# Performance work log

Hardware: AMD Instinct MI355X
Metric: run time of the kernel (lower is better)

## Reference

```python
import jax, jax.numpy as jnp
import numpy as np

B, L, D, NLAYERS, MAX_NODES, DEG = 32, 512, 768, 3, 128, 8


def _build_graph():
    rng = np.random.default_rng(0)
    per = rng.integers(-32, 33, size=B // 2)
    sizes = np.concatenate([96 + per, 96 - per]).astype(np.int64)  # sum = 96*B = 3072, each in [64,128]
    N = int(sizes.sum())
    offs = np.concatenate([[0], np.cumsum(sizes)])
    batch = np.repeat(np.arange(B), sizes).astype(np.int64)
    pad_idx = np.zeros((B, MAX_NODES), np.int64)
    pad_mask = np.zeros((B, MAX_NODES), bool)
    src, dst = [], []
    for b in range(B):
        n = int(sizes[b])
        pad_idx[b, :n] = np.arange(offs[b], offs[b] + n)
        pad_mask[b, :n] = True
        src.append(rng.integers(offs[b], offs[b] + n, n * DEG))
        dst.append(rng.integers(offs[b], offs[b] + n, n * DEG))
    return N, batch, pad_idx, pad_mask, np.concatenate(src), np.concatenate(dst)


def setup_inputs() -> dict:
    N, batch, pad_idx, pad_mask, esrc, edst = _build_graph()
    key = jax.random.key(0)
    ks = jax.random.split(key, 8)
    s = 1.0 / np.sqrt(D)
    return {
        "x": jax.random.normal(ks[0], (N, D), jnp.float32),
        "text": jax.random.normal(ks[1], (B, L, D), jnp.float32),
        "batch_ent1_d_mask": jnp.ones((B, 1), jnp.float32),
        "batch_ent1_g_mask": jnp.ones((B, 1), jnp.float32),
        "gnn_ws": jax.random.normal(ks[2], (NLAYERS, D, D), jnp.float32) * s,
        "gnn_wn": jax.random.normal(ks[3], (NLAYERS, D, D), jnp.float32) * s,
        "gnn_b": jnp.zeros((NLAYERS, D), jnp.float32),
        "atom_w": jax.random.normal(ks[4], (D, D), jnp.float32) * s,
        "atom_b": jnp.zeros((D,), jnp.float32),
        "rand_emb": jax.random.normal(ks[5], (1, D), jnp.float32),
        "batch": jnp.asarray(batch),
        "pad_idx": jnp.asarray(pad_idx),
        "pad_mask": jnp.asarray(pad_mask),
        "edge_src": jnp.asarray(esrc),
        "edge_dst": jnp.asarray(edst),
    }


def reference(x, text, batch_ent1_d_mask, batch_ent1_g_mask, gnn_ws, gnn_wn, gnn_b,
              atom_w, atom_b, rand_emb, batch, pad_idx, pad_mask, edge_src, edge_dst):
    N = x.shape[0]
    E = edge_src.shape[0]
    maskf = pad_mask.astype(x.dtype)            # [B, M]
    n_per = maskf.sum(axis=1)                   # [B] num real nodes per graph
    # edge-neighbor mean counts (constants w.r.t. x)
    cnt = jax.ops.segment_sum(jnp.ones((E,), x.dtype), edge_dst, num_segments=N)
    inv_cnt = 1.0 / jnp.maximum(cnt, 1.0)
    cms = []
    for i in range(NLAYERS):
        # MoleGraphConv stand-in: mean neighbor aggregation + self transform
        msg = jax.ops.segment_sum(x[edge_src], edge_dst, num_segments=N) * inv_cnt[:, None]
        x = jax.nn.relu(x @ gnn_ws[i] + msg @ gnn_wn[i] + gnn_b[i])
        # ragged gather into padded [B, M, D]
        xp = x[pad_idx] * maskf[..., None]
        # graph -> text cross attention (softmax over text tokens; no mask needed)
        g2t = jax.nn.softmax(jnp.einsum('bmd,bld->bml', xp, text), axis=-1)
        g2t_out = jnp.einsum('bml,bld->bmd', g2t, text)            # [B, M, D]
        # text -> graph cross attention (mask padded nodes)
        t2g_logits = jnp.einsum('bld,bmd->blm', text, xp)
        t2g_logits = jnp.where(pad_mask[:, None, :], t2g_logits, jnp.float32(-1e9))
        t2g = jax.nn.softmax(t2g_logits, axis=-1)
        t2g_out = jnp.einsum('blm,bmd->bld', t2g, xp)              # [B, L, D]
        # mean over concatenated rows [n_i + L] per graph (pool_type=2)
        pooled = ((g2t_out * maskf[..., None]).sum(axis=1) + t2g_out.sum(axis=1)) \
                 / (n_per + jnp.float32(L))[:, None]
        cms.append(pooled)
    out_cms = jnp.mean(jnp.stack(cms, axis=1), axis=1)              # mean over layers
    out_t = text[:, 0, :]
    # scatter-mean of final node features per graph
    gsum = jax.ops.segment_sum(x, batch, num_segments=B)
    gcnt = jax.ops.segment_sum(jnp.ones((N,), x.dtype), batch, num_segments=B)
    xg = gsum / jnp.maximum(gcnt, 1.0)[:, None]
    # dropout is a no-op in eval mode
    out_g = jnp.tanh(xg @ atom_w + atom_b)
    z = rand_emb[0]
    dg = batch_ent1_d_mask * batch_ent1_g_mask
    return jnp.concatenate([
        out_t * batch_ent1_d_mask + (1 - batch_ent1_d_mask) * z,
        out_g * batch_ent1_g_mask + (1 - batch_ent1_g_mask) * z,
        out_cms * dg + (1 - dg) * z,
    ], axis=-1)
```

## Files before the change

### kernel.cpp

```cpp
#include <hip/hip_runtime.h>

#define D 768
#define B 32
#define L 512
#define M 128
#define NNODES 3072
#define NEDGES 24576

using bf16x8 = __attribute__((ext_vector_type(8))) short;
using f32x4  = __attribute__((ext_vector_type(4))) float;

__device__ __forceinline__ float bf2f(unsigned short u) {
  union { unsigned int i; float f; } v; v.i = ((unsigned int)u) << 16; return v.f;
}
__device__ __forceinline__ unsigned short f2bf(float f) {
  union { float f; unsigned int i; } v; v.f = f;
  unsigned int x = v.i;
  return (unsigned short)((x + 0x7FFFu + ((x >> 16) & 1u)) >> 16);
}
__device__ __forceinline__ float ldf(const void* p, size_t i, int f32) {
  return f32 ? ((const float*)p)[i] : bf2f(((const unsigned short*)p)[i]);
}
__device__ __forceinline__ int ldi(const void* p, size_t i, int w64) {
  return w64 ? (int)((const long long*)p)[i] : ((const int*)p)[i];
}
__device__ __forceinline__ f32x4 mfma16(bf16x8 a, bf16x8 b, f32x4 c) {
  return __builtin_amdgcn_mfma_f32_16x16x32_bf16(a, b, c, 0, 0, 0);
}
__device__ __forceinline__ void gl_lds(const unsigned short* gsrc, unsigned short* lbase,
                                       int lane) {
  __builtin_amdgcn_global_load_lds(
      (const __attribute__((address_space(1))) unsigned int*)(gsrc + lane * 8),
      (__attribute__((address_space(3))) unsigned int*)lbase, 16, 0, 0);
}

__device__ __forceinline__ float pk_read(const unsigned short* P, int p, int l, int d) {
  return bf2f(P[(((size_t)(p * 24 + (d >> 5))) << 9) + ((((d & 31) >> 3) << 4) + l) * 8 + (d & 7)]);
}

__device__ __forceinline__ void fma8(float* acc, float w, uint4 v) {
  unsigned xs[4] = {v.x, v.y, v.z, v.w};
#pragma unroll
  for (int j = 0; j < 4; ++j) {
    acc[2 * j]     += w * bf2f((unsigned short)(xs[j] & 0xFFFFu));
    acc[2 * j + 1] += w * bf2f((unsigned short)(xs[j] >> 16));
  }
}

__device__ __forceinline__ void acc12(float* a, const uint2* u) {
#pragma unroll
  for (int j = 0; j < 3; ++j) {
    a[j * 4 + 0] += bf2f((unsigned short)(u[j].x & 0xFFFFu));
    a[j * 4 + 1] += bf2f((unsigned short)(u[j].x >> 16));
    a[j * 4 + 2] += bf2f((unsigned short)(u[j].y & 0xFFFFu));
    a[j * 4 + 3] += bf2f((unsigned short)(u[j].y >> 16));
  }
}


__device__ void d_pack_in(const void* src, unsigned short* rows, unsigned short* dst,
                          int p, int tid, int f) {
  unsigned short* pb = dst + (size_t)p * 12288;
  uint4 qv[6];
  if (f) {
    float4 v0[6], v1[6];
#pragma unroll
    for (int j = 0; j < 6; ++j) {
      int odx = j * 256 + tid;
      int kk = odx >> 6, lanep = odx & 63;
      size_t sbase = (size_t)(p * 16 + (lanep & 15)) * 768 + kk * 32 + ((lanep >> 4) << 3);
      const float* sp = (const float*)src + sbase;
      v0[j] = *(const float4*)sp;
      v1[j] = *(const float4*)(sp + 4);
    }
#pragma unroll
    for (int j = 0; j < 6; ++j) {
      union { unsigned short v[8]; uint4 q; } u;
      u.v[0] = f2bf(v0[j].x); u.v[1] = f2bf(v0[j].y); u.v[2] = f2bf(v0[j].z); u.v[3] = f2bf(v0[j].w);
      u.v[4] = f2bf(v1[j].x); u.v[5] = f2bf(v1[j].y); u.v[6] = f2bf(v1[j].z); u.v[7] = f2bf(v1[j].w);
      qv[j] = u.q;
    }
  } else {
#pragma unroll
    for (int j = 0; j < 6; ++j) {
      int odx = j * 256 + tid;
      int kk = odx >> 6, lanep = odx & 63;
      size_t sbase = (size_t)(p * 16 + (lanep & 15)) * 768 + kk * 32 + ((lanep >> 4) << 3);
      qv[j] = *(const uint4*)((const unsigned short*)src + sbase);
    }
  }
#pragma unroll
  for (int j = 0; j < 6; ++j) {
    int odx = j * 256 + tid;
    int kk = odx >> 6, lanep = odx & 63;
    size_t sbase = (size_t)(p * 16 + (lanep & 15)) * 768 + kk * 32 + ((lanep >> 4) << 3);
    if (rows) *(uint4*)&rows[sbase] = qv[j];
    *(uint4*)&pb[(size_t)odx * 8] = qv[j];
  }
}

__device__ void d_pack(const unsigned short* src, unsigned short* dst,
                       int p, int tid) {
  unsigned short* pb = dst + (size_t)p * 12288;
  uint4 qv[6];
#pragma unroll
  for (int j = 0; j < 6; ++j) {
    int odx = j * 256 + tid;
    int kk = odx >> 6, lanep = odx & 63;
    size_t sbase = (size_t)(p * 16 + (lanep & 15)) * 768 + kk * 32 + ((lanep >> 4) << 3);
    qv[j] = *(const uint4*)(src + sbase);
  }
#pragma unroll
  for (int j = 0; j < 6; ++j) {
    *(uint4*)&pb[(size_t)(j * 256 + tid) * 8] = qv[j];
  }
}

__device__ void d_wpack(const void* Ws, const void* Wn, const void* Aw, int f,
                        unsigned short* WsPk, unsigned short* WnPk, unsigned short* AwPk,
                        int r0, int tid) {
  int z = r0 / 288, rem = r0 % 288;
  int nblk = rem % 12, kk = rem / 12;
  const void* src; unsigned short* dst; size_t zoff;
  if (z < 3)      { src = Ws; zoff = (size_t)z * D * D;       dst = WsPk + zoff; }
  else if (z < 6) { src = Wn; zoff = (size_t)(z - 3) * D * D; dst = WnPk + zoff; }
  else            { src = Aw; zoff = 0;                       dst = AwPk; }
  int pl = tid >> 6, lane = tid & 63;
  int pG = nblk * 4 + pl;
  int k0 = kk * 32 + ((lane >> 4) << 3);
  int n  = nblk * 64 + pl * 16 + (lane & 15);
  union { unsigned short v[8]; uint4 q; } u;
  if (f) {
    const float* sp = (const float*)src + zoff + (size_t)k0 * D + n;
#pragma unroll
    for (int e = 0; e < 8; ++e) u.v[e] = f2bf(sp[(size_t)e * D]);
  } else {
    const unsigned short* sp = (const unsigned short*)src + zoff + (size_t)k0 * D + n;
#pragma unroll
    for (int e = 0; e < 8; ++e) u.v[e] = sp[(size_t)e * D];
  }
  *(uint4*)&dst[(((size_t)(pG * 24 + kk)) << 9) + lane * 8] = u.q;
}

__device__ void d_count(const void* edst, const void* batch, int w,
                        int* cnt, int* gcnt, int i) {
  if (i < NEDGES) atomicAdd(&cnt[ldi(edst, i, w)], 1);
  if (i < NNODES) atomicAdd(&gcnt[ldi(batch, i, w)], 1);
}

__device__ void d_msg(const unsigned short* x, const int* cnt, const int* rowstart,
                      const int* csr, unsigned short* Mpk, int p, int tid) {
  int w = tid >> 6, lane = tid & 63;
  unsigned short* pb = Mpk + (size_t)p * 12288;
#pragma unroll
  for (int i = 0; i < 4; i += 2) {
    int rA = w * 4 + i, rB = rA + 1;
    int nA = p * 16 + rA, nB = p * 16 + rB;
    int degA = cnt[nA], baseA = rowstart[nA];
    int degB = cnt[nB], baseB = rowstart[nB];
    float aA[12], aB[12];
#pragma unroll
    for (int j = 0; j < 12; ++j) { aA[j] = 0.f; aB[j] = 0.f; }
    int dmax = degA > degB ? degA : degB;
    for (int e = 0; e < dmax; ++e) {
      uint2 uA[3], uB[3];
      if (e < degA) {
        const uint2* xr = (const uint2*)(x + (size_t)csr[baseA + e] * D);
        uA[0] = xr[lane]; uA[1] = xr[lane + 64]; uA[2] = xr[lane + 128];
      }
      if (e < degB) {
        const uint2* xr = (const uint2*)(x + (size_t)csr[baseB + e] * D);
        uB[0] = xr[lane]; uB[1] = xr[lane + 64]; uB[2] = xr[lane + 128];
      }
      if (e < degA) acc12(aA, uA);
      if (e < degB) acc12(aB, uB);
    }
    float invA = 1.0f / (float)(degA > 1 ? degA : 1);
    float invB = 1.0f / (float)(degB > 1 ? degB : 1);
#pragma unroll
    for (int j = 0; j < 3; ++j) {
      int d0 = (lane + j * 64) * 4;
      int kk = d0 >> 5, q = (d0 >> 3) & 3, e0 = d0 & 7;
      uint2 wA, wB;
      wA.x = (unsigned int)f2bf(aA[j * 4 + 0] * invA)
           | ((unsigned int)f2bf(aA[j * 4 + 1] * invA) << 16);
      wA.y = (unsigned int)f2bf(aA[j * 4 + 2] * invA)
           | ((unsigned int)f2bf(aA[j * 4 + 3] * invA) << 16);
      wB.x = (unsigned int)f2bf(aB[j * 4 + 0] * invB)
           | ((unsigned int)f2bf(aB[j * 4 + 1] * invB) << 16);
      wB.y = (unsigned int)f2bf(aB[j * 4 + 2] * invB)
           | ((unsigned int)f2bf(aB[j * 4 + 3] * invB) << 16);
      *(uint2*)&pb[kk * 512 + (q * 16 + rA) * 8 + e0] = wA;
      *(uint2*)&pb[kk * 512 + (q * 16 + rB) * 8 + e0] = wB;
    }
  }
}

__device__ void d_gemm(const unsigned short* Xpk, const unsigned short* Mpk,
                       const unsigned short* WsPk, const unsigned short* WnPk,
                       const void* bias, size_t bias_off, int f,
                       unsigned short* Y, int bx, int by, int tid, char* smem) {
  unsigned short* lds = (unsigned short*)smem;
  int wave = tid >> 6, lane = tid & 63;
  int q = lane >> 4, t = lane & 15;
  int wm = wave >> 1, wn = wave & 1;
  int pa = bx * 4, pb = by * 4;
  f32x4 acc[2][2];
#pragma unroll
  for (int mi = 0; mi < 2; ++mi)
#pragma unroll
    for (int ni = 0; ni < 2; ++ni)
      acc[mi][ni] = (f32x4){0.f, 0.f, 0.f, 0.f};
  int c0 = wave * 2;
  int pan0 = (wave < 2) ? (pa + c0) : (pb + c0 - 4);
  auto issue = [&](int r) {
    unsigned short* dbuf = &lds[(r % 3) * 8192 + c0 * 512];
#pragma unroll
    for (int st = 0; st < 2; ++st) {
      int s = r * 2 + st;
      int h = (s >= 24) ? 1 : 0;
      const unsigned short* P = (wave < 2) ? (h ? Mpk : Xpk) : (h ? WnPk : WsPk);
      int kk = s - h * 24;
      gl_lds(P + (((size_t)(pan0 * 24 + kk)) << 9), dbuf + st * 4096, lane);
      gl_lds(P + (((size_t)((pan0 + 1) * 24 + kk)) << 9), dbuf + st * 4096 + 512, lane);
    }
  };
  issue(0);
  issue(1);
  for (int r = 0; r < 24; ++r) {
    if (r < 23) asm volatile("s_waitcnt vmcnt(4)" ::: "memory");
    else        asm volatile("s_waitcnt vmcnt(0)" ::: "memory");
    __builtin_amdgcn_s_barrier();
    asm volatile("" ::: "memory");
    if (r < 22) issue(r + 2);
    const unsigned short* bb = &lds[(r % 3) * 8192];
#pragma unroll
    for (int st = 0; st < 2; ++st) {
      const unsigned short* bs = bb + st * 4096;
      bf16x8 a0 = *(const bf16x8*)&bs[(wm * 2 + 0) * 512 + lane * 8];
      bf16x8 a1 = *(const bf16x8*)&bs[(wm * 2 + 1) * 512 + lane * 8];
      bf16x8 b0 = *(const bf16x8*)&bs[(4 + wn * 2 + 0) * 512 + lane * 8];
      bf16x8 b1 = *(const bf16x8*)&bs[(4 + wn * 2 + 1) * 512 + lane * 8];
      acc[0][0] = mfma16(a0, b0, acc[0][0]);
      acc[0][1] = mfma16(a0, b1, acc[0][1]);
      acc[1][0] = mfma16(a1, b0, acc[1][0]);
      acc[1][1] = mfma16(a1, b1, acc[1][1]);
    }
    asm volatile("" ::: "memory");
  }
#pragma unroll
  for (int ni = 0; ni < 2; ++ni) {
    int col = by * 64 + wn * 32 + ni * 16 + t;
    float bv = ldf(bias, bias_off + col, f);
#pragma unroll
    for (int mi = 0; mi < 2; ++mi) {
#pragma unroll
      for (int r = 0; r < 4; ++r) {
        int row = bx * 64 + wm * 32 + mi * 16 + q * 4 + r;
        float v = acc[mi][ni][r] + bv;
        Y[(size_t)row * D + col] = f2bf(v > 0.f ? v : 0.f);
      }
    }
  }
}

__device__ void d_xp(const unsigned short* Xn, const void* pidx, int w64,
                     const int* gcnt, unsigned short* xp, unsigned short* XpPk,
                     float* xgacc, int p, int tid, char* smem) {
  unsigned short* rows = (unsigned short*)smem;
  int r = tid >> 4, c16 = tid & 15;
  int bm = p * 16 + r;
  int b = bm >> 7, m = bm & 127;
  int nb = gcnt[b];
  uint4* dl = (uint4*)&rows[r * 776];
  uint4 v[6];
  if (m < nb) {
    const uint4* srcr = (const uint4*)(Xn + (size_t)ldi(pidx, bm, w64) * D);
#pragma unroll
    for (int j = 0; j < 6; ++j) v[j] = srcr[c16 + j * 16];
  } else {
    uint4 z = {0u, 0u, 0u, 0u};
#pragma unroll
    for (int j = 0; j < 6; ++j) v[j] = z;
  }
#pragma unroll
  for (int j = 0; j < 6; ++j) dl[c16 + j * 16] = v[j];
  __syncthreads();
#pragma unroll
  for (int j = 0; j < 6; ++j) {
    int idx = j * 256 + tid;
    int rr = idx / 96, cc = idx % 96;
    uint4 vv = *(const uint4*)&rows[rr * 776 + cc * 8];
    *(uint4*)&xp[(size_t)(p * 16 + rr) * D + cc * 8] = vv;
  }
  unsigned short* pb = XpPk + (size_t)p * 12288;
#pragma unroll
  for (int j = 0; j < 6; ++j) {
    int odx = j * 256 + tid;
    int kk = odx >> 6, lanep = odx & 63;
    int rr = lanep & 15, cg = lanep >> 4;
    int cc = kk * 4 + cg;
    uint4 vv = *(const uint4*)&rows[rr * 776 + cc * 8];
    *(uint4*)&pb[odx * 8] = vv;
  }
  if (xgacc) {
    int bb = p >> 3;
#pragma unroll
    for (int j = 0; j < 3; ++j) {
      int d = j * 256 + tid;
      float s = 0.f;
#pragma unroll
      for (int rr = 0; rr < 16; ++rr) s += bf2f(rows[rr * 776 + d]);
      atomicAdd(&xgacc[(size_t)bb * D + d], s);
    }
  }
}

__device__ void d_scores(const unsigned short* XpPk, const unsigned short* Tpk,
                         float* S, int bx, int by, int bz, int tid, char* smem) {
  unsigned short* lds = (unsigned short*)smem;
  int wave = tid >> 6, lane = tid & 63;
  int q = lane >> 4, t = lane & 15;
  int wm = wave >> 1, wn = wave & 1;
  int pa = bz * 8 + bx * 4;
  int pb = bz * 32 + by * 4;
  f32x4 acc[2][2];
#pragma unroll
  for (int mi = 0; mi < 2; ++mi)
#pragma unroll
    for (int ni = 0; ni < 2; ++ni)
      acc[mi][ni] = (f32x4){0.f, 0.f, 0.f, 0.f};
  int c0 = wave * 2;
  const unsigned short* P = (wave < 2) ? XpPk : Tpk;
  int pan0 = (wave < 2) ? (pa + c0) : (pb + c0 - 4);
  auto issue = [&](int r) {
    unsigned short* dbuf = &lds[(r % 3) * 8192 + c0 * 512];
#pragma unroll
    for (int st = 0; st < 2; ++st) {
      int kk = r * 2 + st;
      gl_lds(P + (((size_t)(pan0 * 24 + kk)) << 9), dbuf + st * 4096, lane);
      gl_lds(P + (((size_t)((pan0 + 1) * 24 + kk)) << 9), dbuf + st * 4096 + 512, lane);
    }
  };
  issue(0);
  issue(1);
  for (int r = 0; r < 12; ++r) {
    if (r < 11) asm volatile("s_waitcnt vmcnt(4)" ::: "memory");
    else        asm volatile("s_waitcnt vmcnt(0)" ::: "memory");
    __builtin_amdgcn_s_barrier();
    asm volatile("" ::: "memory");
    if (r < 10) issue(r + 2);
    const unsigned short* bb = &lds[(r % 3) * 8192];
#pragma unroll
    for (int st = 0; st < 2; ++st) {
      const unsigned short* bs = bb + st * 4096;
      bf16x8 a0 = *(const bf16x8*)&bs[(wm * 2 + 0) * 512 + lane * 8];
      bf16x8 a1 = *(const bf16x8*)&bs[(wm * 2 + 1) * 512 + lane * 8];
      bf16x8 b0 = *(const bf16x8*)&bs[(4 + wn * 2 + 0) * 512 + lane * 8];
      bf16x8 b1 = *(const bf16x8*)&bs[(4 + wn * 2 + 1) * 512 + lane * 8];
      acc[0][0] = mfma16(a0, b0, acc[0][0]);
      acc[0][1] = mfma16(a0, b1, acc[0][1]);
      acc[1][0] = mfma16(a1, b0, acc[1][0]);
      acc[1][1] = mfma16(a1, b1, acc[1][1]);
    }
    asm volatile("" ::: "memory");
  }
  float* Sb = S + (size_t)bz * M * L;
#pragma unroll
  for (int ni = 0; ni < 2; ++ni) {
    int col = by * 64 + wn * 32 + ni * 16 + t;
#pragma unroll
    for (int mi = 0; mi < 2; ++mi) {
#pragma unroll
      for (int r = 0; r < 4; ++r) {
        int row = bx * 64 + wm * 32 + mi * 16 + q * 4 + r;
        Sb[(size_t)row * L + col] = acc[mi][ni][r];
      }
    }
  }
}

__device__ void d_stats(const float* S, const int* gcnt, float* rmax, float* rsum,
                        float* cmaxv, float* csumv, int bid, int tid, char* smem) {
  if (bid < B * M) {
    float* red = (float*)smem;
    int lane = tid & 63, wv = tid >> 6;
    const float* r = S + (size_t)bid * L;
    float s0 = r[tid], s1 = r[tid + 256];
    float m = fmaxf(s0, s1);
#pragma unroll
    for (int o = 32; o > 0; o >>= 1) m = fmaxf(m, __shfl_down(m, o));
    if (lane == 0) red[wv] = m;
    __syncthreads();
    float bm = fmaxf(fmaxf(red[0], red[1]), fmaxf(red[2], red[3]));
    __syncthreads();
    float e = __expf(s0 - bm) + __expf(s1 - bm);
#pragma unroll
    for (int o = 32; o > 0; o >>= 1) e += __shfl_down(e, o);
    if (lane == 0) red[wv] = e;
    __syncthreads();
    if (tid == 0) { rmax[bid] = bm; rsum[bid] = red[0] + red[1] + red[2] + red[3]; }
  } else {
    float (*pm)[64] = (float(*)[64])smem;
    float (*ps)[64] = (float(*)[64])(smem + 1024);
    int cid = bid - B * M;
    int b = cid >> 3, ly = cid & 7;
    int w = tid >> 6, lane = tid & 63;
    int l = ly * 64 + lane;
    int nb = gcnt[b];
    const float* Sb = S + (size_t)b * M * L;
    int m0 = w * 32, m1 = min(m0 + 32, nb);
    float cm = -1e30f, cs = 0.f;
    for (int m = m0; m < m1; ++m) {
      float s = Sb[(size_t)m * L + l];
      if (s > cm) { cs = cs * __expf(cm - s) + 1.f; cm = s; }
      else cs += __expf(s - cm);
    }
    pm[w][lane] = cm; ps[w][lane] = cs;
    __syncthreads();
    if (w == 0) {
      float CM = -1e30f;
#pragma unroll
      for (int j = 0; j < 4; ++j) CM = fmaxf(CM, pm[j][lane]);
      float CS = 0.f;
#pragma unroll
      for (int j = 0; j < 4; ++j) CS += ps[j][lane] * __expf(pm[j][lane] - CM);
      cmaxv[b * L + l] = CM; csumv[b * L + l] = CS;
    }
  }
}

__device__ void d_cross(const float* S, const float* rmax, const float* rsum,
                        const float* cmaxv, const float* csumv, const int* gcnt,
                        float* wv, float* t2gcol, int bid, int tid, char* smem) {
  if (bid < 256) {
    float* rm = (float*)smem;
    float* ri = (float*)(smem + 512);
    float (*pw)[64] = (float(*)[64])(smem + 1024);
    int b = bid >> 3, ly = bid & 7;
    int w = tid >> 6, lane = tid & 63;
    if (tid < M) { rm[tid] = rmax[b * M + tid]; ri[tid] = 1.f / rsum[b * M + tid]; }
    __syncthreads();
    int l = ly * 64 + lane;
    int nb = gcnt[b];
    const float* Sb = S + (size_t)b * M * L;
    int m0 = w * 32, m1 = min(m0 + 32, nb);
    float wp = 0.f;
    for (int m = m0; m < m1; ++m)
      wp += __expf(Sb[(size_t)m * L + l] - rm[m]) * ri[m];
    pw[w][lane] = wp;
    __syncthreads();
    if (w == 0)
      wv[b * L + l] = pw[0][lane] + pw[1][lane] + pw[2][lane] + pw[3][lane];
  } else {
    float* red = (float*)smem;
    int bm = bid - 256;
    int b = bm >> 7, m = bm & 127;
    int lane = tid & 63, w = tid >> 6;
    int nb = gcnt[b];
    float acc = 0.f;
    if (m < nb) {
      const float* r = S + (size_t)bm * L;
      const float* cm = cmaxv + b * L;
      const float* cs = csumv + b * L;
      acc = __expf(r[tid] - cm[tid]) / cs[tid]
          + __expf(r[tid + 256] - cm[tid + 256]) / cs[tid + 256];
    }
#pragma unroll
    for (int o = 32; o > 0; o >>= 1) acc += __shfl_down(acc, o);
    if (lane == 0) red[w] = acc;
    __syncthreads();
    if (tid == 0) t2gcol[bm] = red[0] + red[1] + red[2] + red[3];
  }
}

__device__ void d_pooled(const float* wv, const float* t2gcol, const unsigned short* Tpk,
                         const unsigned short* xp, const int* gcnt, float* pooled,
                         int bid, int tid, char* smem) {
  float* lred = (float*)smem;
  float* wbuf = (float*)(smem + 3072);
  int b = bid / 10, seg = bid - b * 10;
  int chunk = tid % 96, half = tid / 96;
  int d = chunk * 8;
  float acc[8];
#pragma unroll
  for (int j = 0; j < 8; ++j) acc[j] = 0.f;
  if (tid < 64) {
    wbuf[tid] = (seg < 8) ? wv[b * L + seg * 64 + tid]
                          : t2gcol[b * M + (seg - 8) * 64 + tid];
  }
  __syncthreads();
  if (half < 2) {
    if (seg < 8) {
      int pbase = b * 32 + seg * 4;
      size_t cbase = ((size_t)(d >> 5)) << 9;
      int coff = ((d & 31) >> 3) << 4;
      for (int i = 0; i < 32; ++i) {
        int l = half * 32 + i;
        const unsigned short* src =
            Tpk + (((size_t)((pbase + (l >> 4)) * 24)) << 9) + cbase +
            (size_t)(coff + (l & 15)) * 8;
        fma8(acc, wbuf[l], *(const uint4*)src);
      }
    } else {
      const unsigned short* Xb = xp + (size_t)b * M * D + d;
      int m0 = (seg - 8) * 64;
      for (int i = 0; i < 32; ++i) {
        int mm = half * 32 + i;
        fma8(acc, wbuf[mm], *(const uint4*)&Xb[(size_t)(m0 + mm) * D]);
      }
    }
  }
  if (half == 1) {
#pragma unroll
    for (int j = 0; j < 8; ++j) lred[chunk * 8 + j] = acc[j];
  }
  __syncthreads();
  if (half == 0) {
    float inv = 1.f / ((float)gcnt[b] + 512.f);
#pragma unroll
    for (int j = 0; j < 8; ++j)
      atomicAdd(&pooled[(size_t)b * D + d + j], (acc[j] + lred[chunk * 8 + j]) * inv);
  }
}

__device__ void d_atom(const float* xgacc, const int* gcnt, const unsigned short* AwPk,
                       float* gpre, int bid, int tid) {
  int w = tid >> 6, lane = tid & 63;
  int q = lane >> 4, t = lane & 15;
  int nbase = bid * 64 + w * 16;
  int pb = nbase >> 4;
  int n0 = gcnt[t], n1 = gcnt[16 + t];
  float inv0 = 1.f / (float)(n0 > 1 ? n0 : 1);
  float inv1 = 1.f / (float)(n1 > 1 ? n1 : 1);
  f32x4 acc[2];
  acc[0] = (f32x4){0.f, 0.f, 0.f, 0.f};
  acc[1] = (f32x4){0.f, 0.f, 0.f, 0.f};
  for (int kk = 0; kk < 24; ++kk) {
    const float* s0 = xgacc + (size_t)t * D + kk * 32 + q * 8;
    const float* s1 = xgacc + (size_t)(16 + t) * D + kk * 32 + q * 8;
    union { unsigned short v[8]; bf16x8 f; } a0, a1;
#pragma unroll
    for (int j = 0; j < 8; ++j) { a0.v[j] = f2bf(s0[j] * inv0); a1.v[j] = f2bf(s1[j] * inv1); }
    bf16x8 bv = *(const bf16x8*)(AwPk + (((size_t)(pb * 24 + kk)) << 9) + (lane << 3));
    acc[0] = mfma16(a0.f, bv, acc[0]);
    acc[1] = mfma16(a1.f, bv, acc[1]);
  }
#pragma unroll
  for (int mi = 0; mi < 2; ++mi)
#pragma unroll
    for (int r = 0; r < 4; ++r) {
      int row = mi * 16 + q * 4 + r;
      gpre[(size_t)row * D + nbase + t] = acc[mi][r];
    }
}


__global__ void k_init(int* cnt, int* cursor, int* gcnt, float* pooled, float* xgacc,
                       const unsigned short* __restrict__ t,
                       const unsigned int* __restrict__ e, int* __restrict__ flags) {
  int i = blockIdx.x * 256 + threadIdx.x;
  if (i < NNODES) { cnt[i] = 0; cursor[i] = 0; }
  if (i < B) gcnt[i] = 0;
  if (i < B * D) { pooled[i] = 0.f; xgacc[i] = 0.f; }
  if (blockIdx.x == 0) {
    __shared__ int r0[256];
    __shared__ unsigned r1[256];
    int tid = threadIdx.x;
    int bad = 0;
    for (int j = tid; j < 8192; j += 256) {
      unsigned short u = t[2 * j];
      unsigned ex = (u >> 7) & 0xFF;
      if (ex >= 0xC0) bad = 1;
    }
    unsigned o = 0;
    for (int j = tid; j < NEDGES / 2; j += 256) o |= e[2 * j + 1];
    r0[tid] = bad; r1[tid] = o;
    __syncthreads();
    for (int s = 128; s > 0; s >>= 1) {
      if (tid < s) { r0[tid] |= r0[tid + s]; r1[tid] |= r1[tid + s]; }
      __syncthreads();
    }
    if (tid == 0) { flags[0] = r0[0]; flags[1] = (r1[0] == 0) ? 1 : 0; }
  }
}

__global__ __launch_bounds__(256) void k_setup2(
    const void* x_in, unsigned short* x0, unsigned short* PkA,
    const void* text, unsigned short* Tpk,
    const void* Ws, const void* Wn, const void* Aw,
    unsigned short* WsPk, unsigned short* WnPk, unsigned short* AwPk,
    const void* edst, const void* batch, int* cnt, int* gcnt,
    const int* __restrict__ flags) {
  int bid = blockIdx.x, tid = threadIdx.x;
  if (bid < 1216) {
    int f = flags[0];
    if (bid < NNODES / 16) d_pack_in(x_in, x0, PkA, bid, tid, f);
    else d_pack_in(text, nullptr, Tpk, bid - NNODES / 16, tid, f);
  } else if (bid < 3232) {
    d_wpack(Ws, Wn, Aw, flags[0], WsPk, WnPk, AwPk, bid - 1216, tid);
  } else {
    d_count(edst, batch, flags[1], cnt, gcnt, (bid - 3232) * 256 + tid);
  }
}

__global__ void k_scan(const int* __restrict__ cnt, int* __restrict__ rowstart) {
  __shared__ int a[NNODES], b[NNODES];
  int tid = threadIdx.x;
  for (int i = tid; i < NNODES; i += 1024) a[i] = cnt[i];
  __syncthreads();
  int* s = a; int* d = b;
  for (int off = 1; off < NNODES; off <<= 1) {
    for (int i = tid; i < NNODES; i += 1024)
      d[i] = s[i] + (i >= off ? s[i - off] : 0);
    __syncthreads();
    int* t = s; s = d; d = t;
  }
  for (int i = tid; i < NNODES; i += 1024) rowstart[i + 1] = s[i];
  if (tid == 0) rowstart[0] = 0;
}

__global__ void k_scatter(const void* __restrict__ esrc, const void* __restrict__ edst,
                          const int* __restrict__ flags, const int* __restrict__ rowstart,
                          int* __restrict__ cursor, int* __restrict__ csr) {
  int w = flags[1];
  int i = blockIdx.x * 256 + threadIdx.x;
  if (i < NEDGES) {
    int dd = ldi(edst, i, w);
    int pos = atomicAdd(&cursor[dd], 1);
    csr[rowstart[dd] + pos] = ldi(esrc, i, w);
  }
}

__global__ __launch_bounds__(256) void k_msgp(
    const unsigned short* x, const int* cnt, const int* rowstart, const int* csr,
    unsigned short* Mpk) {
  d_msg(x, cnt, rowstart, csr, Mpk, blockIdx.x, threadIdx.x);
}

__device__ __forceinline__ void gemm_map(int g, int& bx, int& by) {
  int gs = (g % 8) * 72 + g / 8;
  bx = gs / 12; by = gs % 12;
}
__device__ __forceinline__ void sc_map(int g, int& bx, int& by, int& bz) {
  int gs = (g % 8) * 64 + g / 8;
  bx = gs & 1; by = (gs >> 1) & 7; bz = gs >> 4;
}

__global__ __launch_bounds__(256) void k_gemm(
    const unsigned short* Apk, const unsigned short* Mpk,
    const unsigned short* WsPk, const unsigned short* WnPk,
    const void* bias, unsigned long bias_off, const int* flags, unsigned short* Y) {
  extern __shared__ char smem[];
  int bx, by; gemm_map(blockIdx.x, bx, by);
  d_gemm(Apk, Mpk, WsPk, WnPk, bias, bias_off, flags[0], Y, bx, by,
         threadIdx.x, smem);
}

__global__ __launch_bounds__(256) void k_postg(
    const unsigned short* Y, unsigned short* Npk, int packN,
    const void* pidx, const int* flags, const int* gcnt,
    unsigned short* xp, unsigned short* XpPk, float* xgacc) {
  extern __shared__ char smem[];
  int bid = blockIdx.x, tid = threadIdx.x;
  if (bid < 256) d_xp(Y, pidx, flags[1], gcnt, xp, XpPk, xgacc, bid, tid, smem);
  else d_pack(Y, Npk, bid - 256, tid);
}

__global__ __launch_bounds__(256) void k_scmsg(
    const unsigned short* XpPk, const unsigned short* Tpk, float* S,
    int msgN, const unsigned short* x, const int* cnt, const int* rowstart,
    const int* csr, unsigned short* Mpk) {
  extern __shared__ char smem[];
  int bid = blockIdx.x, tid = threadIdx.x;
  if (bid < msgN) d_msg(x, cnt, rowstart, csr, Mpk, bid, tid);
  else {
    int bx, by, bz; sc_map(bid - msgN, bx, by, bz);
    d_scores(XpPk, Tpk, S, bx, by, bz, tid, smem);
  }
}

__global__ __launch_bounds__(256) void k_stgemm(
    const float* S, const int* gcnt, float* rmax, float* rsum, float* cmaxv, float* csumv,
    int gemmN, const unsigned short* Apk, const unsigned short* Mpk,
    const unsigned short* WsPk, const unsigned short* WnPk,
    const void* bias, unsigned long bias_off, const int* flags, unsigned short* Y) {
  extern __shared__ char smem[];
  int bid = blockIdx.x, tid = threadIdx.x;
  if (bid < gemmN) {
    int bx, by; gemm_map(bid, bx, by);
    d_gemm(Apk, Mpk, WsPk, WnPk, bias, bias_off, flags[0], Y, bx, by, tid, smem);
  } else d_stats(S, gcnt, rmax, rsum, cmaxv, csumv, bid - gemmN, tid, smem);
}

__global__ __launch_bounds__(256) void k_crpostg(
    const float* S, const float* rmax, const float* rsum, const float* cmaxv,
    const float* csumv, const int* gcnt, float* wv, float* t2gcol,
    int packN, int xpN, const unsigned short* Y, unsigned short* Npk,
    const void* pidx, const int* flags, unsigned short* xp, unsigned short* XpPk,
    float* xgacc) {
  extern __shared__ char smem[];
  int bid = blockIdx.x, tid = threadIdx.x;
  if (bid < packN) { d_pack(Y, Npk, bid, tid); return; }
  int r = bid - packN;
  if (r < xpN) { d_xp(Y, pidx, flags[1], gcnt, xp, XpPk, xgacc, r, tid, smem); return; }
  d_cross(S, rmax, rsum, cmaxv, csumv, gcnt, wv, t2gcol, r - xpN, tid, smem);
}

__global__ __launch_bounds__(256) void k_plscmsg(
    const float* wv, const float* t2gcol, const unsigned short* Tpk,
    const unsigned short* xpL, const int* gcnt, float* pooled,
    int scN, const unsigned short* XpPk, float* S,
    int msgN, const unsigned short* x, const int* cnt, const int* rowstart,
    const int* csr, unsigned short* Mpk,
    int atomN, const float* xgacc, const unsigned short* AwPk, float* gpre) {
  extern __shared__ char smem[];
  int bid = blockIdx.x, tid = threadIdx.x;
  if (bid < msgN) { d_msg(x, cnt, rowstart, csr, Mpk, bid, tid); return; }
  int r = bid - msgN;
  if (r < scN) {
    int bx, by, bz; sc_map(r, bx, by, bz);
    d_scores(XpPk, Tpk, S, bx, by, bz, tid, smem); return;
  }
  r -= scN;
  if (r < 320) { d_pooled(wv, t2gcol, Tpk, xpL, gcnt, pooled, r, tid, smem); return; }
  d_atom(xgacc, gcnt, AwPk, gpre, r - 320, tid);
}

__global__ __launch_bounds__(256) void k_final(
    const unsigned short* __restrict__ Tpk, const float* __restrict__ gpre,
    const float* __restrict__ pooled, const void* __restrict__ ab,
    const void* __restrict__ dmask, const void* __restrict__ gmask,
    const void* __restrict__ remb, const int* __restrict__ flags,
    void* __restrict__ out) {
  int f = flags[0];
  int b = blockIdx.x, tid = threadIdx.x;
  float dm = ldf(dmask, b, f);
  float gm = ldf(gmask, b, f);
  float dg = dm * gm;
  size_t base = (size_t)b * 2304;
#pragma unroll
  for (int j = 0; j < 3; ++j) {
    int d = tid + j * 256;
    float z = ldf(remb, d, f);
    float tv = pk_read(Tpk, b * 32, 0, d);
    float o0 = tv * dm + (1.f - dm) * z;
    float gv = tanhf(gpre[(size_t)b * D + d] + ldf(ab, d, f));
    float o1 = gv * gm + (1.f - gm) * z;
    float p = pooled[(size_t)b * D + d] * (1.f / 3.f);
    float o2 = p * dg + (1.f - dg) * z;
    if (f) {
      float* of = (float*)out;
      of[base + d] = o0; of[base + 768 + d] = o1; of[base + 1536 + d] = o2;
    } else {
      unsigned short* ob = (unsigned short*)out;
      ob[base + d] = f2bf(o0); ob[base + 768 + d] = f2bf(o1); ob[base + 1536 + d] = f2bf(o2);
    }
  }
}

extern "C" void kernel_launch(void* const* d_in, const int* in_sizes, int n_in,
                              void* d_out, int out_size, void* d_ws, size_t ws_size,
                              hipStream_t stream) {
  const void* x_in  = d_in[0];
  const void* text  = d_in[1];
  const void* dmask = d_in[2];
  const void* gmask = d_in[3];
  const void* gws   = d_in[4];
  const void* gwn   = d_in[5];
  const void* gb    = d_in[6];
  const void* aw    = d_in[7];
  const void* ab    = d_in[8];
  const void* remb  = d_in[9];
  const void* batch = d_in[10];
  const void* pidx  = d_in[11];
  const void* esrc  = d_in[13];
  const void* edst  = d_in[14];

  char* wsp = (char*)d_ws;
  size_t off = 0;
  auto carve = [&](size_t bytes) -> void* {
    void* p = wsp + off;
    off += (bytes + 255) & ~(size_t)255;
    return p;
  };
  int* flags = (int*)carve(2 * 4);
  unsigned short* x0    = (unsigned short*)carve((size_t)NNODES * D * 2);
  unsigned short* xA    = (unsigned short*)carve((size_t)NNODES * D * 2);
  unsigned short* xB    = (unsigned short*)carve((size_t)NNODES * D * 2);
  unsigned short* PkA   = (unsigned short*)carve((size_t)NNODES * D * 2);
  unsigned short* PkB   = (unsigned short*)carve((size_t)NNODES * D * 2);
  unsigned short* Mpk   = (unsigned short*)carve((size_t)NNODES * D * 2);
  unsigned short* Tpk   = (unsigned short*)carve((size_t)B * L * D * 2);
  unsigned short* WsPk  = (unsigned short*)carve((size_t)3 * D * D * 2);
  unsigned short* WnPk  = (unsigned short*)carve((size_t)3 * D * D * 2);
  unsigned short* AwPk  = (unsigned short*)carve((size_t)D * D * 2);
  unsigned short* xpA   = (unsigned short*)carve((size_t)B * M * D * 2);
  unsigned short* xpB   = (unsigned short*)carve((size_t)B * M * D * 2);
  unsigned short* XpPkA = (unsigned short*)carve((size_t)B * M * D * 2);
  unsigned short* XpPkB = (unsigned short*)carve((size_t)B * M * D * 2);
  float* xgacc   = (float*)carve((size_t)B * D * 4);
  float* gpre    = (float*)carve((size_t)B * D * 4);
  float* S       = (float*)carve((size_t)B * M * L * 4);
  float* rmax    = (float*)carve((size_t)B * M * 4);
  float* rsum    = (float*)carve((size_t)B * M * 4);
  float* wv      = (float*)carve((size_t)B * L * 4);
  float* cmaxv   = (float*)carve((size_t)B * L * 4);
  float* csumv   = (float*)carve((size_t)B * L * 4);
  float* t2gcol  = (float*)carve((size_t)B * M * 4);
  float* pooled  = (float*)carve((size_t)B * D * 4);
  int* cnt      = (int*)carve((size_t)NNODES * 4);
  int* rowstart = (int*)carve((size_t)(NNODES + 1) * 4);
  int* cursor   = (int*)carve((size_t)NNODES * 4);
  int* gcnt     = (int*)carve((size_t)B * 4);
  int* csr      = (int*)carve((size_t)NEDGES * 4);

  const size_t DD = (size_t)D * D;

  k_init<<<96, 256, 0, stream>>>(cnt, cursor, gcnt, pooled, xgacc,
                                 (const unsigned short*)text, (const unsigned int*)edst, flags);
  k_setup2<<<3328, 256, 0, stream>>>(x_in, x0, PkA, text, Tpk, gws, gwn, aw,
                                     WsPk, WnPk, AwPk, edst, batch, cnt, gcnt, flags);
  k_scan<<<1, 1024, 0, stream>>>(cnt, rowstart);
  k_scatter<<<96, 256, 0, stream>>>(esrc, edst, flags, rowstart, cursor, csr);

  k_msgp<<<192, 256, 0, stream>>>(x0, cnt, rowstart, csr, Mpk);
  k_gemm<<<576, 256, 49152, stream>>>(PkA, Mpk, WsPk, WnPk, gb, 0, flags, xA);
  k_postg<<<448, 256, 24832, stream>>>(xA, PkB, 192, pidx, flags, gcnt, xpA, XpPkA, nullptr);
  k_scmsg<<<704, 256, 49152, stream>>>(XpPkA, Tpk, S, 192, xA, cnt, rowstart, csr, Mpk);
  k_stgemm<<<4928, 256, 49152, stream>>>(S, gcnt, rmax, rsum, cmaxv, csumv,
                                         576, PkB, Mpk, WsPk + DD, WnPk + DD, gb, D, flags, xB);
  k_crpostg<<<4800, 256, 24832, stream>>>(S, rmax, rsum, cmaxv, csumv, gcnt, wv, t2gcol,
                                          192, 256, xB, PkA, pidx, flags, xpB, XpPkB, nullptr);
  k_plscmsg<<<1024, 256, 49152, stream>>>(wv, t2gcol, Tpk, xpA, gcnt, pooled,
                                          512, XpPkB, S, 192, xB, cnt, rowstart, csr, Mpk,
                                          0, nullptr, nullptr, nullptr);
  k_stgemm<<<4928, 256, 49152, stream>>>(S, gcnt, rmax, rsum, cmaxv, csumv,
                                         576, PkA, Mpk, WsPk + 2 * DD, WnPk + 2 * DD,
                                         gb, 2 * D, flags, xA);
  k_crpostg<<<4608, 256, 24832, stream>>>(S, rmax, rsum, cmaxv, csumv, gcnt, wv, t2gcol,
                                          0, 256, xA, nullptr, pidx, flags, xpA, XpPkA, xgacc);
  k_plscmsg<<<832, 256, 49152, stream>>>(wv, t2gcol, Tpk, xpB, gcnt, pooled,
                                         512, XpPkA, S, 0, nullptr, nullptr, nullptr,
                                         nullptr, nullptr, 0, nullptr, nullptr, nullptr);
  k_stgemm<<<4352, 256, 2048, stream>>>(S, gcnt, rmax, rsum, cmaxv, csumv,
                                        0, nullptr, nullptr, nullptr, nullptr,
                                        nullptr, 0, flags, nullptr);
  k_crpostg<<<4352, 256, 2048, stream>>>(S, rmax, rsum, cmaxv, csumv, gcnt, wv, t2gcol,
                                         0, 0, nullptr, nullptr, pidx, flags,
                                         nullptr, nullptr, nullptr);
  k_plscmsg<<<332, 256, 4096, stream>>>(wv, t2gcol, Tpk, xpA, gcnt, pooled,
                                        0, nullptr, nullptr, 0, nullptr, nullptr, nullptr,
                                        nullptr, nullptr, 12, xgacc, AwPk, gpre);
  k_final<<<32, 256, 0, stream>>>(Tpk, gpre, pooled, ab, dmask, gmask, remb, flags, d_out);
}
```

Before: 434.0 us.

## Keep node features only in packed MFMA layout and drop row-major copies

The GEMM epilogue now writes node features straight into the packed tile layout, and message passing, xp gathering and pooling read that packed layout directly. This removes the separate row-major buffers and the d_pack/xp copy blocks, cutting memory traffic and block count in several fused kernels. The GEMM pipelines also move to single-k-step stages with a 6-deep LDS ring and 5 loads in flight. Graph counting uses a wave ballot so each run of equal batch ids does one atomic, and fused kernels reorder their block roles. The trade-off is scattered 2-byte epilogue stores and less contiguous gathers.

Result: slower. 494.5 us (+13.9%).

```diff
diff --git a/kernel.cpp b/kernel.cpp
--- a/kernel.cpp
+++ b/kernel.cpp
@@ -58,8 +58,7 @@
 }
 
 
-__device__ void d_pack_in(const void* src, unsigned short* rows, unsigned short* dst,
-                          int p, int tid, int f) {
+__device__ void d_pack_in(const void* src, unsigned short* dst, int p, int tid, int f) {
   unsigned short* pb = dst + (size_t)p * 12288;
   uint4 qv[6];
   if (f) {
@@ -90,30 +89,8 @@
     }
   }
 #pragma unroll
-  for (int j = 0; j < 6; ++j) {
-    int odx = j * 256 + tid;
-    int kk = odx >> 6, lanep = odx & 63;
-    size_t sbase = (size_t)(p * 16 + (lanep & 15)) * 768 + kk * 32 + ((lanep >> 4) << 3);
-    if (rows) *(uint4*)&rows[sbase] = qv[j];
-    *(uint4*)&pb[(size_t)odx * 8] = qv[j];
-  }
-}
-
-__device__ void d_pack(const unsigned short* src, unsigned short* dst,
-                       int p, int tid) {
-  unsigned short* pb = dst + (size_t)p * 12288;
-  uint4 qv[6];
-#pragma unroll
-  for (int j = 0; j < 6; ++j) {
-    int odx = j * 256 + tid;
-    int kk = odx >> 6, lanep = odx & 63;
-    size_t sbase = (size_t)(p * 16 + (lanep & 15)) * 768 + kk * 32 + ((lanep >> 4) << 3);
-    qv[j] = *(const uint4*)(src + sbase);
-  }
-#pragma unroll
-  for (int j = 0; j < 6; ++j) {
+  for (int j = 0; j < 6; ++j)
     *(uint4*)&pb[(size_t)(j * 256 + tid) * 8] = qv[j];
-  }
 }
 
 __device__ void d_wpack(const void* Ws, const void* Wn, const void* Aw, int f,
@@ -145,13 +122,30 @@
 __device__ void d_count(const void* edst, const void* batch, int w,
                         int* cnt, int* gcnt, int i) {
   if (i < NEDGES) atomicAdd(&cnt[ldi(edst, i, w)], 1);
-  if (i < NNODES) atomicAdd(&gcnt[ldi(batch, i, w)], 1);
-}
-
-__device__ void d_msg(const unsigned short* x, const int* cnt, const int* rowstart,
+  if (i < NNODES) {
+    int b = ldi(batch, i, w);
+    int lane = i & 63;
+    int prev = __shfl_up(b, 1);
+    bool first = (lane == 0) || (prev != b);
+    unsigned long long bm = __ballot(first ? 1 : 0);
+    if (first) {
+      unsigned long long higher = (lane < 63) ? (bm >> (lane + 1)) : 0ULL;
+      int next = higher ? (lane + __ffsll((long long)higher)) : 64;
+      atomicAdd(&gcnt[b], next - lane);
+    }
+  }
+}
+
+__device__ void d_msg(const unsigned short* Px, const int* cnt, const int* rowstart,
                       const int* csr, unsigned short* Mpk, int p, int tid) {
   int w = tid >> 6, lane = tid & 63;
   unsigned short* pb = Mpk + (size_t)p * 12288;
+  int koff[3];
+#pragma unroll
+  for (int j = 0; j < 3; ++j) {
+    int k0 = (lane + j * 64) * 4;
+    koff[j] = (k0 >> 5) * 512 + ((k0 >> 3) & 3) * 128 + (k0 & 7);
+  }
 #pragma unroll
   for (int i = 0; i < 4; i += 2) {
     int rA = w * 4 + i, rB = rA + 1;
@@ -165,12 +159,18 @@
     for (int e = 0; e < dmax; ++e) {
       uint2 uA[3], uB[3];
       if (e < degA) {
-        const uint2* xr = (const uint2*)(x + (size_t)csr[baseA + e] * D);
-        uA[0] = xr[lane]; uA[1] = xr[lane + 64]; uA[2] = xr[lane + 128];
+        int n = csr[baseA + e];
+        const unsigned short* gb = Px + (size_t)(n >> 4) * 12288 + (n & 15) * 8;
+        uA[0] = *(const uint2*)(gb + koff[0]);
+        uA[1] = *(const uint2*)(gb + koff[1]);
+        uA[2] = *(const uint2*)(gb + koff[2]);
       }
       if (e < degB) {
-        const uint2* xr = (const uint2*)(x + (size_t)csr[baseB + e] * D);
-        uB[0] = xr[lane]; uB[1] = xr[lane + 64]; uB[2] = xr[lane + 128];
+        int n = csr[baseB + e];
+        const unsigned short* gb = Px + (size_t)(n >> 4) * 12288 + (n & 15) * 8;
+        uB[0] = *(const uint2*)(gb + koff[0]);
+        uB[1] = *(const uint2*)(gb + koff[1]);
+        uB[2] = *(const uint2*)(gb + koff[2]);
       }
       if (e < degA) acc12(aA, uA);
       if (e < degB) acc12(aB, uB);
@@ -179,8 +179,6 @@
     float invB = 1.0f / (float)(degB > 1 ? degB : 1);
 #pragma unroll
     for (int j = 0; j < 3; ++j) {
-      int d0 = (lane + j * 64) * 4;
-      int kk = d0 >> 5, q = (d0 >> 3) & 3, e0 = d0 & 7;
       uint2 wA, wB;
       wA.x = (unsigned int)f2bf(aA[j * 4 + 0] * invA)
            | ((unsigned int)f2bf(aA[j * 4 + 1] * invA) << 16);
@@ -190,8 +188,8 @@
            | ((unsigned int)f2bf(aB[j * 4 + 1] * invB) << 16);
       wB.y = (unsigned int)f2bf(aB[j * 4 + 2] * invB)
            | ((unsigned int)f2bf(aB[j * 4 + 3] * invB) << 16);
-      *(uint2*)&pb[kk * 512 + (q * 16 + rA) * 8 + e0] = wA;
-      *(uint2*)&pb[kk * 512 + (q * 16 + rB) * 8 + e0] = wB;
+      *(uint2*)&pb[koff[j] + rA * 8] = wA;
+      *(uint2*)&pb[koff[j] + rB * 8] = wB;
     }
   }
 }
@@ -199,12 +197,12 @@
 __device__ void d_gemm(const unsigned short* Xpk, const unsigned short* Mpk,
                        const unsigned short* WsPk, const unsigned short* WnPk,
                        const void* bias, size_t bias_off, int f,
-                       unsigned short* Y, int bx, int by, int tid, char* smem) {
+                       unsigned short* Ypk, int bx, int by, int tid, char* smem) {
   unsigned short* lds = (unsigned short*)smem;
   int wave = tid >> 6, lane = tid & 63;
   int q = lane >> 4, t = lane & 15;
   int wm = wave >> 1, wn = wave & 1;
-  int pa = bx * 4, pb = by * 4;
+  int pa = bx * 4, pbp = by * 4;
   f32x4 acc[2][2];
 #pragma unroll
   for (int mi = 0; mi < 2; ++mi)
@@ -212,60 +210,54 @@
     for (int ni = 0; ni < 2; ++ni)
       acc[mi][ni] = (f32x4){0.f, 0.f, 0.f, 0.f};
   int c0 = wave * 2;
-  int pan0 = (wave < 2) ? (pa + c0) : (pb + c0 - 4);
-  auto issue = [&](int r) {
-    unsigned short* dbuf = &lds[(r % 3) * 8192 + c0 * 512];
-#pragma unroll
-    for (int st = 0; st < 2; ++st) {
-      int s = r * 2 + st;
-      int h = (s >= 24) ? 1 : 0;
-      const unsigned short* P = (wave < 2) ? (h ? Mpk : Xpk) : (h ? WnPk : WsPk);
-      int kk = s - h * 24;
-      gl_lds(P + (((size_t)(pan0 * 24 + kk)) << 9), dbuf + st * 4096, lane);
-      gl_lds(P + (((size_t)((pan0 + 1) * 24 + kk)) << 9), dbuf + st * 4096 + 512, lane);
-    }
+  int pan0 = (wave < 2) ? (pa + c0) : (pbp + c0 - 4);
+  auto issue = [&](int s) {
+    int h = (s >= 24) ? 1 : 0;
+    const unsigned short* P = (wave < 2) ? (h ? Mpk : Xpk) : (h ? WnPk : WsPk);
+    int kk = s - h * 24;
+    unsigned short* dbuf = &lds[(s % 6) * 4096 + c0 * 512];
+    gl_lds(P + (((size_t)(pan0 * 24 + kk)) << 9), dbuf, lane);
+    gl_lds(P + (((size_t)((pan0 + 1) * 24 + kk)) << 9), dbuf + 512, lane);
   };
-  issue(0);
-  issue(1);
-  for (int r = 0; r < 24; ++r) {
-    if (r < 23) asm volatile("s_waitcnt vmcnt(4)" ::: "memory");
+#pragma unroll
+  for (int s = 0; s < 5; ++s) issue(s);
+  for (int r = 0; r < 48; ++r) {
+    if (r < 44) asm volatile("s_waitcnt vmcnt(8)" ::: "memory");
     else        asm volatile("s_waitcnt vmcnt(0)" ::: "memory");
     __builtin_amdgcn_s_barrier();
     asm volatile("" ::: "memory");
-    if (r < 22) issue(r + 2);
-    const unsigned short* bb = &lds[(r % 3) * 8192];
-#pragma unroll
-    for (int st = 0; st < 2; ++st) {
-      const unsigned short* bs = bb + st * 4096;
-      bf16x8 a0 = *(const bf16x8*)&bs[(wm * 2 + 0) * 512 + lane * 8];
-      bf16x8 a1 = *(const bf16x8*)&bs[(wm * 2 + 1) * 512 + lane * 8];
-      bf16x8 b0 = *(const bf16x8*)&bs[(4 + wn * 2 + 0) * 512 + lane * 8];
-      bf16x8 b1 = *(const bf16x8*)&bs[(4 + wn * 2 + 1) * 512 + lane * 8];
-      acc[0][0] = mfma16(a0, b0, acc[0][0]);
-      acc[0][1] = mfma16(a0, b1, acc[0][1]);
-      acc[1][0] = mfma16(a1, b0, acc[1][0]);
-      acc[1][1] = mfma16(a1, b1, acc[1][1]);
-    }
+    if (r + 5 < 48) issue(r + 5);
+    const unsigned short* bs = &lds[(r % 6) * 4096];
+    bf16x8 a0 = *(const bf16x8*)&bs[(wm * 2 + 0) * 512 + lane * 8];
+    bf16x8 a1 = *(const bf16x8*)&bs[(wm * 2 + 1) * 512 + lane * 8];
+    bf16x8 b0 = *(const bf16x8*)&bs[(4 + wn * 2 + 0) * 512 + lane * 8];
+    bf16x8 b1 = *(const bf16x8*)&bs[(4 + wn * 2 + 1) * 512 + lane * 8];
+    acc[0][0] = mfma16(a0, b0, acc[0][0]);
+    acc[0][1] = mfma16(a0, b1, acc[0][1]);
+    acc[1][0] = mfma16(a1, b0, acc[1][0]);
+    acc[1][1] = mfma16(a1, b1, acc[1][1]);
     asm volatile("" ::: "memory");
   }
 #pragma unroll
   for (int ni = 0; ni < 2; ++ni) {
     int col = by * 64 + wn * 32 + ni * 16 + t;
     float bv = ldf(bias, bias_off + col, f);
+    int kkc = col >> 5, cq = (col >> 3) & 3, ec = col & 7;
 #pragma unroll
     for (int mi = 0; mi < 2; ++mi) {
+      int pOut = bx * 4 + wm * 2 + mi;
+      unsigned short* ob = Ypk + (size_t)pOut * 12288 + kkc * 512 + ec;
 #pragma unroll
       for (int r = 0; r < 4; ++r) {
-        int row = bx * 64 + wm * 32 + mi * 16 + q * 4 + r;
         float v = acc[mi][ni][r] + bv;
-        Y[(size_t)row * D + col] = f2bf(v > 0.f ? v : 0.f);
+        ob[(cq * 16 + q * 4 + r) * 8] = f2bf(v > 0.f ? v : 0.f);
       }
     }
   }
 }
 
-__device__ void d_xp(const unsigned short* Xn, const void* pidx, int w64,
-                     const int* gcnt, unsigned short* xp, unsigned short* XpPk,
+__device__ void d_xp(const unsigned short* PkN, const void* pidx, int w64,
+                     const int* gcnt, unsigned short* XpPk,
                      float* xgacc, int p, int tid, char* smem) {
   unsigned short* rows = (unsigned short*)smem;
   int r = tid >> 4, c16 = tid & 15;
@@ -275,9 +267,13 @@
   uint4* dl = (uint4*)&rows[r * 776];
   uint4 v[6];
   if (m < nb) {
-    const uint4* srcr = (const uint4*)(Xn + (size_t)ldi(pidx, bm, w64) * D);
-#pragma unroll
-    for (int j = 0; j < 6; ++j) v[j] = srcr[c16 + j * 16];
+    int n = ldi(pidx, bm, w64);
+    const unsigned short* base = PkN + (size_t)(n >> 4) * 12288 + (n & 15) * 8;
+#pragma unroll
+    for (int j = 0; j < 6; ++j) {
+      int mg = c16 + j * 16;
+      v[j] = *(const uint4*)(base + (mg >> 2) * 512 + (mg & 3) * 128);
+    }
   } else {
     uint4 z = {0u, 0u, 0u, 0u};
 #pragma unroll
@@ -286,13 +282,6 @@
 #pragma unroll
   for (int j = 0; j < 6; ++j) dl[c16 + j * 16] = v[j];
   __syncthreads();
-#pragma unroll
-  for (int j = 0; j < 6; ++j) {
-    int idx = j * 256 + tid;
-    int rr = idx / 96, cc = idx % 96;
-    uint4 vv = *(const uint4*)&rows[rr * 776 + cc * 8];
-    *(uint4*)&xp[(size_t)(p * 16 + rr) * D + cc * 8] = vv;
-  }
   unsigned short* pb = XpPk + (size_t)p * 12288;
 #pragma unroll
   for (int j = 0; j < 6; ++j) {
@@ -323,7 +312,7 @@
   int q = lane >> 4, t = lane & 15;
   int wm = wave >> 1, wn = wave & 1;
   int pa = bz * 8 + bx * 4;
-  int pb = bz * 32 + by * 4;
+  int pbp = bz * 32 + by * 4;
   f32x4 acc[2][2];
 #pragma unroll
   for (int mi = 0; mi < 2; ++mi)
@@ -332,37 +321,29 @@
       acc[mi][ni] = (f32x4){0.f, 0.f, 0.f, 0.f};
   int c0 = wave * 2;
   const unsigned short* P = (wave < 2) ? XpPk : Tpk;
-  int pan0 = (wave < 2) ? (pa + c0) : (pb + c0 - 4);
-  auto issue = [&](int r) {
-    unsigned short* dbuf = &lds[(r % 3) * 8192 + c0 * 512];
-#pragma unroll
-    for (int st = 0; st < 2; ++st) {
-      int kk = r * 2 + st;
-      gl_lds(P + (((size_t)(pan0 * 24 + kk)) << 9), dbuf + st * 4096, lane);
-      gl_lds(P + (((size_t)((pan0 + 1) * 24 + kk)) << 9), dbuf + st * 4096 + 512, lane);
-    }
+  int pan0 = (wave < 2) ? (pa + c0) : (pbp + c0 - 4);
+  auto issue = [&](int kk) {
+    unsigned short* dbuf = &lds[(kk % 6) * 4096 + c0 * 512];
+    gl_lds(P + (((size_t)(pan0 * 24 + kk)) << 9), dbuf, lane);
+    gl_lds(P + (((size_t)((pan0 + 1) * 24 + kk)) << 9), dbuf + 512, lane);
   };
-  issue(0);
-  issue(1);
-  for (int r = 0; r < 12; ++r) {
-    if (r < 11) asm volatile("s_waitcnt vmcnt(4)" ::: "memory");
+#pragma unroll
+  for (int s = 0; s < 5; ++s) issue(s);
+  for (int r = 0; r < 24; ++r) {
+    if (r < 20) asm volatile("s_waitcnt vmcnt(8)" ::: "memory");
     else        asm volatile("s_waitcnt vmcnt(0)" ::: "memory");
     __builtin_amdgcn_s_barrier();
     asm volatile("" ::: "memory");
-    if (r < 10) issue(r + 2);
-    const unsigned short* bb = &lds[(r % 3) * 8192];
-#pragma unroll
-    for (int st = 0; st < 2; ++st) {
-      const unsigned short* bs = bb + st * 4096;
-      bf16x8 a0 = *(const bf16x8*)&bs[(wm * 2 + 0) * 512 + lane * 8];
-      bf16x8 a1 = *(const bf16x8*)&bs[(wm * 2 + 1) * 512 + lane * 8];
-      bf16x8 b0 = *(const bf16x8*)&bs[(4 + wn * 2 + 0) * 512 + lane * 8];
-      bf16x8 b1 = *(const bf16x8*)&bs[(4 + wn * 2 + 1) * 512 + lane * 8];
-      acc[0][0] = mfma16(a0, b0, acc[0][0]);
-      acc[0][1] = mfma16(a0, b1, acc[0][1]);
-      acc[1][0] = mfma16(a1, b0, acc[1][0]);
-      acc[1][1] = mfma16(a1, b1, acc[1][1]);
-    }
+    if (r + 5 < 24) issue(r + 5);
+    const unsigned short* bs = &lds[(r % 6) * 4096];
+    bf16x8 a0 = *(const bf16x8*)&bs[(wm * 2 + 0) * 512 + lane * 8];
+    bf16x8 a1 = *(const bf16x8*)&bs[(wm * 2 + 1) * 512 + lane * 8];
+    bf16x8 b0 = *(const bf16x8*)&bs[(4 + wn * 2 + 0) * 512 + lane * 8];
+    bf16x8 b1 = *(const bf16x8*)&bs[(4 + wn * 2 + 1) * 512 + lane * 8];
+    acc[0][0] = mfma16(a0, b0, acc[0][0]);
+    acc[0][1] = mfma16(a0, b1, acc[0][1]);
+    acc[1][0] = mfma16(a1, b0, acc[1][0]);
+    acc[1][1] = mfma16(a1, b1, acc[1][1]);
     asm volatile("" ::: "memory");
   }
   float* Sb = S + (size_t)bz * M * L;
@@ -475,7 +456,7 @@
 }
 
 __device__ void d_pooled(const float* wv, const float* t2gcol, const unsigned short* Tpk,
-                         const unsigned short* xp, const int* gcnt, float* pooled,
+                         const unsigned short* XpPk, const int* gcnt, float* pooled,
                          int bid, int tid, char* smem) {
   float* lred = (float*)smem;
   float* wbuf = (float*)(smem + 3072);
@@ -491,23 +472,25 @@
   }
   __syncthreads();
   if (half < 2) {
+    size_t cbase = ((size_t)(d >> 5)) << 9;
+    int coff = ((d & 31) >> 3) << 4;
     if (seg < 8) {
       int pbase = b * 32 + seg * 4;
-      size_t cbase = ((size_t)(d >> 5)) << 9;
-      int coff = ((d & 31) >> 3) << 4;
       for (int i = 0; i < 32; ++i) {
         int l = half * 32 + i;
         const unsigned short* src =
-            Tpk + (((size_t)((pbase + (l >> 4)) * 24)) << 9) + cbase +
-            (size_t)(coff + (l & 15)) * 8;
+            Tpk + (size_t)(pbase + (l >> 4)) * 12288 + cbase + (size_t)(coff + (l & 15)) * 8;
         fma8(acc, wbuf[l], *(const uint4*)src);
       }
     } else {
-      const unsigned short* Xb = xp + (size_t)b * M * D + d;
+      const unsigned short* Xb = XpPk + (size_t)b * 8 * 12288;
       int m0 = (seg - 8) * 64;
       for (int i = 0; i < 32; ++i) {
         int mm = half * 32 + i;
-        fma8(acc, wbuf[mm], *(const uint4*)&Xb[(size_t)(m0 + mm) * D]);
+        int node = m0 + mm;
+        const unsigned short* src =
+            Xb + (size_t)(node >> 4) * 12288 + cbase + (size_t)(coff + (node & 15)) * 8;
+        fma8(acc, wbuf[mm], *(const uint4*)src);
       }
     }
   }
@@ -586,7 +569,7 @@
 }
 
 __global__ __launch_bounds__(256) void k_setup2(
-    const void* x_in, unsigned short* x0, unsigned short* PkA,
+    const void* x_in, unsigned short* Pk0,
     const void* text, unsigned short* Tpk,
     const void* Ws, const void* Wn, const void* Aw,
     unsigned short* WsPk, unsigned short* WnPk, unsigned short* AwPk,
@@ -595,8 +578,8 @@
   int bid = blockIdx.x, tid = threadIdx.x;
   if (bid < 1216) {
     int f = flags[0];
-    if (bid < NNODES / 16) d_pack_in(x_in, x0, PkA, bid, tid, f);
-    else d_pack_in(text, nullptr, Tpk, bid - NNODES / 16, tid, f);
+    if (bid < NNODES / 16) d_pack_in(x_in, Pk0, bid, tid, f);
+    else d_pack_in(text, Tpk, bid - NNODES / 16, tid, f);
   } else if (bid < 3232) {
     d_wpack(Ws, Wn, Aw, flags[0], WsPk, WnPk, AwPk, bid - 1216, tid);
   } else {
@@ -633,9 +616,9 @@
 }
 
 __global__ __launch_bounds__(256) void k_msgp(
-    const unsigned short* x, const int* cnt, const int* rowstart, const int* csr,
+    const unsigned short* Px, const int* cnt, const int* rowstart, const int* csr,
     unsigned short* Mpk) {
-  d_msg(x, cnt, rowstart, csr, Mpk, blockIdx.x, threadIdx.x);
+  d_msg(Px, cnt, rowstart, csr, Mpk, blockIdx.x, threadIdx.x);
 }
 
 __device__ __forceinline__ void gemm_map(int g, int& bx, int& by) {
@@ -650,81 +633,75 @@
 __global__ __launch_bounds__(256) void k_gemm(
     const unsigned short* Apk, const unsigned short* Mpk,
     const unsigned short* WsPk, const unsigned short* WnPk,
-    const void* bias, unsigned long bias_off, const int* flags, unsigned short* Y) {
+    const void* bias, unsigned long bias_off, const int* flags, unsigned short* Ypk) {
   extern __shared__ char smem[];
   int bx, by; gemm_map(blockIdx.x, bx, by);
-  d_gemm(Apk, Mpk, WsPk, WnPk, bias, bias_off, flags[0], Y, bx, by,
+  d_gemm(Apk, Mpk, WsPk, WnPk, bias, bias_off, flags[0], Ypk, bx, by,
          threadIdx.x, smem);
 }
 
 __global__ __launch_bounds__(256) void k_postg(
-    const unsigned short* Y, unsigned short* Npk, int packN,
-    const void* pidx, const int* flags, const int* gcnt,
-    unsigned short* xp, unsigned short* XpPk, float* xgacc) {
+    const unsigned short* PkN, const void* pidx, const int* flags, const int* gcnt,
+    unsigned short* XpPk, float* xgacc) {
   extern __shared__ char smem[];
-  int bid = blockIdx.x, tid = threadIdx.x;
-  if (bid < 256) d_xp(Y, pidx, flags[1], gcnt, xp, XpPk, xgacc, bid, tid, smem);
-  else d_pack(Y, Npk, bid - 256, tid);
+  d_xp(PkN, pidx, flags[1], gcnt, XpPk, xgacc, blockIdx.x, threadIdx.x, smem);
 }
 
 __global__ __launch_bounds__(256) void k_scmsg(
     const unsigned short* XpPk, const unsigned short* Tpk, float* S,
-    int msgN, const unsigned short* x, const int* cnt, const int* rowstart,
+    int msgN, const unsigned short* Px, const int* cnt, const int* rowstart,
     const int* csr, unsigned short* Mpk) {
   extern __shared__ char smem[];
   int bid = blockIdx.x, tid = threadIdx.x;
-  if (bid < msgN) d_msg(x, cnt, rowstart, csr, Mpk, bid, tid);
-  else {
-    int bx, by, bz; sc_map(bid - msgN, bx, by, bz);
+  if (bid < 512) {
+    int bx, by, bz; sc_map(bid, bx, by, bz);
     d_scores(XpPk, Tpk, S, bx, by, bz, tid, smem);
-  }
+  } else d_msg(Px, cnt, rowstart, csr, Mpk, bid - 512, tid);
 }
 
 __global__ __launch_bounds__(256) void k_stgemm(
     const float* S, const int* gcnt, float* rmax, float* rsum, float* cmaxv, float* csumv,
     int gemmN, const unsigned short* Apk, const unsigned short* Mpk,
     const unsigned short* WsPk, const unsigned short* WnPk,
-    const void* bias, unsigned long bias_off, const int* flags, unsigned short* Y) {
+    const void* bias, unsigned long bias_off, const int* flags, unsigned short* Ypk) {
   extern __shared__ char smem[];
   int bid = blockIdx.x, tid = threadIdx.x;
-  if (bid < gemmN) {
-    int bx, by; gemm_map(bid, bx, by);
-    d_gemm(Apk, Mpk, WsPk, WnPk, bias, bias_off, flags[0], Y, bx, by, tid, smem);
-  } else d_stats(S, gcnt, rmax, rsum, cmaxv, csumv, bid - gemmN, tid, smem);
+  if (bid < 4352) d_stats(S, gcnt, rmax, rsum, cmaxv, csumv, bid, tid, smem);
+  else {
+    int bx, by; gemm_map(bid - 4352, bx, by);
+    d_gemm(Apk, Mpk, WsPk, WnPk, bias, bias_off, flags[0], Ypk, bx, by, tid, smem);
+  }
 }
 
 __global__ __launch_bounds__(256) void k_crpostg(
     const float* S, const float* rmax, const float* rsum, const float* cmaxv,
     const float* csumv, const int* gcnt, float* wv, float* t2gcol,
-    int packN, int xpN, const unsigned short* Y, unsigned short* Npk,
-    const void* pidx, const int* flags, unsigned short* xp, unsigned short* XpPk,
-    float* xgacc) {
+    int xpN, const unsigned short* PkN, const void* pidx, const int* flags,
+    unsigned short* XpPk, float* xgacc) {
   extern __shared__ char smem[];
   int bid = blockIdx.x, tid = threadIdx.x;
-  if (bid < packN) { d_pack(Y, Npk, bid, tid); return; }
-  int r = bid - packN;
-  if (r < xpN) { d_xp(Y, pidx, flags[1], gcnt, xp, XpPk, xgacc, r, tid, smem); return; }
-  d_cross(S, rmax, rsum, cmaxv, csumv, gcnt, wv, t2gcol, r - xpN, tid, smem);
+  if (bid < 4352) d_cross(S, rmax, rsum, cmaxv, csumv, gcnt, wv, t2gcol, bid, tid, smem);
+  else d_xp(PkN, pidx, flags[1], gcnt, XpPk, xgacc, bid - 4352, tid, smem);
 }
 
 __global__ __launch_bounds__(256) void k_plscmsg(
     const float* wv, const float* t2gcol, const unsigned short* Tpk,
-    const unsigned short* xpL, const int* gcnt, float* pooled,
+    const unsigned short* XpPkL, const int* gcnt, float* pooled,
     int scN, const unsigned short* XpPk, float* S,
-    int msgN, const unsigned short* x, const int* cnt, const int* rowstart,
+    int msgN, const unsigned short* Px, const int* cnt, const int* rowstart,
     const int* csr, unsigned short* Mpk,
     int atomN, const float* xgacc, const unsigned short* AwPk, float* gpre) {
   extern __shared__ char smem[];
   int bid = blockIdx.x, tid = threadIdx.x;
-  if (bid < msgN) { d_msg(x, cnt, rowstart, csr, Mpk, bid, tid); return; }
-  int r = bid - msgN;
+  if (bid < 320) { d_pooled(wv, t2gcol, Tpk, XpPkL, gcnt, pooled, bid, tid, smem); return; }
+  int r = bid - 320;
   if (r < scN) {
     int bx, by, bz; sc_map(r, bx, by, bz);
     d_scores(XpPk, Tpk, S, bx, by, bz, tid, smem); return;
   }
   r -= scN;
-  if (r < 320) { d_pooled(wv, t2gcol, Tpk, xpL, gcnt, pooled, r, tid, smem); return; }
-  d_atom(xgacc, gcnt, AwPk, gpre, r - 320, tid);
+  if (r < msgN) { d_msg(Px, cnt, rowstart, csr, Mpk, r, tid); return; }
+  d_atom(xgacc, gcnt, AwPk, gpre, r - msgN, tid);
 }
 
 __global__ __launch_bounds__(256) void k_final(
@@ -785,18 +762,15 @@
     return p;
   };
   int* flags = (int*)carve(2 * 4);
-  unsigned short* x0    = (unsigned short*)carve((size_t)NNODES * D * 2);
-  unsigned short* xA    = (unsigned short*)carve((size_t)NNODES * D * 2);
-  unsigned short* xB    = (unsigned short*)carve((size_t)NNODES * D * 2);
-  unsigned short* PkA   = (unsigned short*)carve((size_t)NNODES * D * 2);
-  unsigned short* PkB   = (unsigned short*)carve((size_t)NNODES * D * 2);
+  unsigned short* Pk0   = (unsigned short*)carve((size_t)NNODES * D * 2);
+  unsigned short* PkN1  = (unsigned short*)carve((size_t)NNODES * D * 2);
+  unsigned short* PkN2  = (unsigned short*)carve((size_t)NNODES * D * 2);
+  unsigned short* PkN3  = (unsigned short*)carve((size_t)NNODES * D * 2);
   unsigned short* Mpk   = (unsigned short*)carve((size_t)NNODES * D * 2);
   unsigned short* Tpk   = (unsigned short*)carve((size_t)B * L * D * 2);
   unsigned short* WsPk  = (unsigned short*)carve((size_t)3 * D * D * 2);
   unsigned short* WnPk  = (unsigned short*)carve((size_t)3 * D * D * 2);
   unsigned short* AwPk  = (unsigned short*)carve((size_t)D * D * 2);
-  unsigned short* xpA   = (unsigned short*)carve((size_t)B * M * D * 2);
-  unsigned short* xpB   = (unsigned short*)carve((size_t)B * M * D * 2);
   unsigned short* XpPkA = (unsigned short*)carve((size_t)B * M * D * 2);
   unsigned short* XpPkB = (unsigned short*)carve((size_t)B * M * D * 2);
   float* xgacc   = (float*)carve((size_t)B * D * 4);
@@ -819,37 +793,36 @@
 
   k_init<<<96, 256, 0, stream>>>(cnt, cursor, gcnt, pooled, xgacc,
                                  (const unsigned short*)text, (const unsigned int*)edst, flags);
-  k_setup2<<<3328, 256, 0, stream>>>(x_in, x0, PkA, text, Tpk, gws, gwn, aw,
+  k_setup2<<<3328, 256, 0, stream>>>(x_in, Pk0, text, Tpk, gws, gwn, aw,
                                      WsPk, WnPk, AwPk, edst, batch, cnt, gcnt, flags);
   k_scan<<<1, 1024, 0, stream>>>(cnt, rowstart);
   k_scatter<<<96, 256, 0, stream>>>(esrc, edst, flags, rowstart, cursor, csr);
 
-  k_msgp<<<192, 256, 0, stream>>>(x0, cnt, rowstart, csr, Mpk);
-  k_gemm<<<576, 256, 49152, stream>>>(PkA, Mpk, WsPk, WnPk, gb, 0, flags, xA);
-  k_postg<<<448, 256, 24832, stream>>>(xA, PkB, 192, pidx, flags, gcnt, xpA, XpPkA, nullptr);
-  k_scmsg<<<704, 256, 49152, stream>>>(XpPkA, Tpk, S, 192, xA, cnt, rowstart, csr, Mpk);
+  k_msgp<<<192, 256, 0, stream>>>(Pk0, cnt, rowstart, csr, Mpk);
+  k_gemm<<<576, 256, 49152, stream>>>(Pk0, Mpk, WsPk, WnPk, gb, 0, flags, PkN1);
+  k_postg<<<256, 256, 24832, stream>>>(PkN1, pidx, flags, gcnt, XpPkA, nullptr);
+  k_scmsg<<<704, 256, 49152, stream>>>(XpPkA, Tpk, S, 192, PkN1, cnt, rowstart, csr, Mpk);
   k_stgemm<<<4928, 256, 49152, stream>>>(S, gcnt, rmax, rsum, cmaxv, csumv,
-                                         576, PkB, Mpk, WsPk + DD, WnPk + DD, gb, D, flags, xB);
-  k_crpostg<<<4800, 256, 24832, stream>>>(S, rmax, rsum, cmaxv, csumv, gcnt, wv, t2gcol,
-                                          192, 256, xB, PkA, pidx, flags, xpB, XpPkB, nullptr);
-  k_plscmsg<<<1024, 256, 49152, stream>>>(wv, t2gcol, Tpk, xpA, gcnt, pooled,
-                                          512, XpPkB, S, 192, xB, cnt, rowstart, csr, Mpk,
+                                         576, PkN1, Mpk, WsPk + DD, WnPk + DD, gb, D, flags, PkN2);
+  k_crpostg<<<4608, 256, 24832, stream>>>(S, rmax, rsum, cmaxv, csumv, gcnt, wv, t2gcol,
+                                          256, PkN2, pidx, flags, XpPkB, nullptr);
+  k_plscmsg<<<1024, 256, 49152, stream>>>(wv, t2gcol, Tpk, XpPkA, gcnt, pooled,
+                                          512, XpPkB, S, 192, PkN2, cnt, rowstart, csr, Mpk,
                                           0, nullptr, nullptr, nullptr);
   k_stgemm<<<4928, 256, 49152, stream>>>(S, gcnt, rmax, rsum, cmaxv, csumv,
-                                         576, PkA, Mpk, WsPk + 2 * DD, WnPk + 2 * DD,
-                                         gb, 2 * D, flags, xA);
+                                         576, PkN2, Mpk, WsPk + 2 * DD, WnPk + 2 * DD,
+                                         gb, 2 * D, flags, PkN3);
   k_crpostg<<<4608, 256, 24832, stream>>>(S, rmax, rsum, cmaxv, csumv, gcnt, wv, t2gcol,
-                                          0, 256, xA, nullptr, pidx, flags, xpA, XpPkA, xgacc);
-  k_plscmsg<<<832, 256, 49152, stream>>>(wv, t2gcol, Tpk, xpB, gcnt, pooled,
+                                          256, PkN3, pidx, flags, XpPkA, xgacc);
+  k_plscmsg<<<832, 256, 49152, stream>>>(wv, t2gcol, Tpk, XpPkB, gcnt, pooled,
                                          512, XpPkA, S, 0, nullptr, nullptr, nullptr,
                                          nullptr, nullptr, 0, nullptr, nullptr, nullptr);
   k_stgemm<<<4352, 256, 2048, stream>>>(S, gcnt, rmax, rsum, cmaxv, csumv,
                                         0, nullptr, nullptr, nullptr, nullptr,
                                         nullptr, 0, flags, nullptr);
   k_crpostg<<<4352, 256, 2048, stream>>>(S, rmax, rsum, cmaxv, csumv, gcnt, wv, t2gcol,
-                                         0, 0, nullptr, nullptr, pidx, flags,
-                                         nullptr, nullptr, nullptr);
-  k_plscmsg<<<332, 256, 4096, stream>>>(wv, t2gcol, Tpk, xpA, gcnt, pooled,
+                                         0, nullptr, pidx, flags, nullptr, nullptr);
+  k_plscmsg<<<332, 256, 4096, stream>>>(wv, t2gcol, Tpk, XpPkA, gcnt, pooled,
                                         0, nullptr, nullptr, 0, nullptr, nullptr, nullptr,
                                         nullptr, nullptr, 12, xgacc, AwPk, gpre);
   k_final<<<32, 256, 0, stream>>>(Tpk, gpre, pooled, ab, dmask, gmask, remb, flags, d_out);
```
